# Performance work log

Hardware: AMD Instinct MI355X
Metric: run time of the kernel (lower is better)

Reference implementation:

```python
import jax, jax.numpy as jnp
import numpy as np

LAMBDA_RECON = 1.0
LAMBDA_IF = 0.5
LAMBDA_SMOOTH = 0.1

B, N, T = 8, 8, 262144


def setup_inputs() -> dict:
    key = jax.random.key(0)
    ks = jax.random.split(key, 7)
    return {
        "recon_real": jax.random.normal(ks[0], (B, T), dtype=jnp.float32),
        "recon_imag": jax.random.normal(ks[1], (B, T), dtype=jnp.float32),
        "target_real": jax.random.normal(ks[2], (B, T), dtype=jnp.float32),
        "target_imag": jax.random.normal(ks[3], (B, T), dtype=jnp.float32),
        "eIF": jax.random.normal(ks[4], (B, N, T), dtype=jnp.float32),
        "target_if": jax.random.normal(ks[5], (B, N, T), dtype=jnp.float32),
        "mode_mask": jax.random.randint(ks[6], (B, N), 0, 2, dtype=jnp.int32),
    }


def _mse(a, b):
    d = a - b
    return jnp.mean(d * d)


def reference(recon_real, recon_imag, target_real, target_imag, eIF, target_if, mode_mask):
    # reconstruction loss: MSE on real part + MSE on imag part
    recon_loss = _mse(recon_real, target_real) + _mse(recon_imag, target_imag)
    total_loss = LAMBDA_RECON * recon_loss

    # IF loss: mask broadcast over time axis, MSE of masked tensors
    maskf = (mode_mask == 1).astype(eIF.dtype)          # [B, N]
    valid = maskf[:, :, None]                            # [B, N, 1] broadcasts over T
    if_loss = _mse(eIF * valid, target_if * valid)
    total_loss = total_loss + LAMBDA_IF * if_loss

    # smoothness: mean of per-(b,n) mean squared temporal diff, over masked modes
    if_diff = eIF[:, :, 1:] - eIF[:, :, :-1]             # [B, N, T-1]
    per_mode = jnp.mean(if_diff * if_diff, axis=-1)      # [B, N]
    count = jnp.sum(maskf)
    smooth_loss = jnp.sum(per_mode * maskf) / jnp.maximum(count, 1.0)
    # original skips smooth term if no mode is active
    smooth_term = jnp.where(count > 0, LAMBDA_SMOOTH * smooth_loss, 0.0)
    total_loss = total_loss + smooth_term

    return total_loss, recon_loss, if_loss, smooth_loss
```

## Files before the change

kernel.cpp:

```cpp
#include <hip/hip_runtime.h>


namespace {
constexpr int    kB = 8;
constexpr int    kN = 8;
constexpr int    kT = 262144;
constexpr long long kBT  = (long long)kB * kT;
constexpr long long kBNT = (long long)kB * kN * kT;

constexpr int THREADS     = 256;
constexpr int RECON_UNITS = 512;
constexpr int SEGS        = 32;
constexpr int IF_UNITS    = kB * kN * SEGS;
constexpr int TOTAL_UNITS = RECON_UNITS + IF_UNITS;
constexpr int GRID        = 1024;

constexpr double LAMBDA_IF     = 0.5;
constexpr double LAMBDA_SMOOTH = 0.1;
}

__device__ __forceinline__ float sq(float x) { return x * x; }

__device__ __forceinline__ void block_reduce2_store(float a, float b, double* dst) {
    double da = (double)a, db = (double)b;
    #pragma unroll
    for (int o = 32; o > 0; o >>= 1) {
        da += __shfl_down(da, o, 64);
        db += __shfl_down(db, o, 64);
    }
    __shared__ double lds[8];
    const int lane = threadIdx.x & 63;
    const int wid  = threadIdx.x >> 6;
    if (lane == 0) { lds[wid] = da; lds[wid + 4] = db; }
    __syncthreads();
    if (threadIdx.x == 0) {
        dst[0] = lds[0] + lds[1] + lds[2] + lds[3];
        dst[1] = lds[4] + lds[5] + lds[6] + lds[7];
    }
    __syncthreads();
}

__global__ __launch_bounds__(THREADS, 4)
void vncmd_main_kernel(const float* __restrict__ rr, const float* __restrict__ ri,
                       const float* __restrict__ tr, const float* __restrict__ ti,
                       const float* __restrict__ eIF, const float* __restrict__ tIF,
                       const int* __restrict__ mask, double* __restrict__ ws) {
    const int tid = threadIdx.x;

    __shared__ int smask[kB * kN];
    if (tid < kB * kN) smask[tid] = mask[tid];
    __syncthreads();

    for (int u = blockIdx.x; u < TOTAL_UNITS; u += GRID) {
        if (u < RECON_UNITS) {
            constexpr int STRIDE = RECON_UNITS * THREADS;
            const int base = u * THREADS + tid;
            const float4* rr4 = (const float4*)rr;
            const float4* tr4 = (const float4*)tr;
            const float4* ri4 = (const float4*)ri;
            const float4* ti4 = (const float4*)ti;
            const int v0 = base, v1 = base + STRIDE, v2 = base + 2 * STRIDE, v3 = base + 3 * STRIDE;

            float4 x0 = rr4[v0], x1 = rr4[v1], x2 = rr4[v2], x3 = rr4[v3];
            float4 y0 = tr4[v0], y1 = tr4[v1], y2 = tr4[v2], y3 = tr4[v3];
            float4 u0 = ri4[v0], u1 = ri4[v1], u2 = ri4[v2], u3 = ri4[v3];
            float4 w0 = ti4[v0], w1 = ti4[v1], w2 = ti4[v2], w3 = ti4[v3];

            float a0 = sq(x0.x - y0.x) + sq(x0.y - y0.y) + sq(x0.z - y0.z) + sq(x0.w - y0.w)
                     + sq(x1.x - y1.x) + sq(x1.y - y1.y) + sq(x1.z - y1.z) + sq(x1.w - y1.w)
                     + sq(x2.x - y2.x) + sq(x2.y - y2.y) + sq(x2.z - y2.z) + sq(x2.w - y2.w)
                     + sq(x3.x - y3.x) + sq(x3.y - y3.y) + sq(x3.z - y3.z) + sq(x3.w - y3.w);
            float a1 = sq(u0.x - w0.x) + sq(u0.y - w0.y) + sq(u0.z - w0.z) + sq(u0.w - w0.w)
                     + sq(u1.x - w1.x) + sq(u1.y - w1.y) + sq(u1.z - w1.z) + sq(u1.w - w1.w)
                     + sq(u2.x - w2.x) + sq(u2.y - w2.y) + sq(u2.z - w2.z) + sq(u2.w - w2.w)
                     + sq(u3.x - w3.x) + sq(u3.y - w3.y) + sq(u3.z - w3.z) + sq(u3.w - w3.w);
            block_reduce2_store(a0, a1, ws + 2 * u);
        } else {
            const int iu  = u - RECON_UNITS;
            const int row = iu >> 5;
            const int seg = iu & (SEGS - 1);
            double* dst = ws + 2 * u;
            if (smask[row] != 1) {
                if (tid == 0) { dst[0] = 0.0; dst[1] = 0.0; }
                continue;
            }

            const float4* e4 = (const float4*)(eIF + (size_t)row * kT);
            const float4* t4 = (const float4*)(tIF + (size_t)row * kT);
            constexpr int VPR = kT / 4;
            constexpr int VPS = 2048;
            const int v0 = seg * VPS + tid;
            const bool lane63 = (tid & 63) == 63;

            float a2 = 0.f, a3 = 0.f;
            #pragma unroll
            for (int h = 0; h < 2; ++h) {
                const int b0 = v0 + (4 * h) * THREADS;
                const int b1 = b0 + THREADS, b2 = b0 + 2 * THREADS, b3 = b0 + 3 * THREADS;
                float4 e0 = e4[b0], e1 = e4[b1], e2 = e4[b2], e3 = e4[b3];
                float4 q0 = t4[b0], q1 = t4[b1], q2 = t4[b2], q3 = t4[b3];
                float n0 = 0.f, n1 = 0.f, n2 = 0.f, n3 = 0.f;
                if (lane63) {
                    n0 = (b0 + 1 < VPR) ? e4[b0 + 1].x : e0.w;
                    n1 = (b1 + 1 < VPR) ? e4[b1 + 1].x : e1.w;
                    n2 = (b2 + 1 < VPR) ? e4[b2 + 1].x : e2.w;
                    n3 = (b3 + 1 < VPR) ? e4[b3 + 1].x : e3.w;
                }
                a2 += sq(e0.x - q0.x) + sq(e0.y - q0.y) + sq(e0.z - q0.z) + sq(e0.w - q0.w)
                    + sq(e1.x - q1.x) + sq(e1.y - q1.y) + sq(e1.z - q1.z) + sq(e1.w - q1.w)
                    + sq(e2.x - q2.x) + sq(e2.y - q2.y) + sq(e2.z - q2.z) + sq(e2.w - q2.w)
                    + sq(e3.x - q3.x) + sq(e3.y - q3.y) + sq(e3.z - q3.z) + sq(e3.w - q3.w);
                a3 += sq(e0.y - e0.x) + sq(e0.z - e0.y) + sq(e0.w - e0.z)
                    + sq(e1.y - e1.x) + sq(e1.z - e1.y) + sq(e1.w - e1.z)
                    + sq(e2.y - e2.x) + sq(e2.z - e2.y) + sq(e2.w - e2.z)
                    + sq(e3.y - e3.x) + sq(e3.z - e3.y) + sq(e3.w - e3.z);
                float s0 = __shfl_down(e0.x, 1, 64);
                float s1 = __shfl_down(e1.x, 1, 64);
                float s2 = __shfl_down(e2.x, 1, 64);
                float s3 = __shfl_down(e3.x, 1, 64);
                if (lane63) { s0 = n0; s1 = n1; s2 = n2; s3 = n3; }
                a3 += sq(s0 - e0.w) + sq(s1 - e1.w) + sq(s2 - e2.w) + sq(s3 - e3.w);
            }
            block_reduce2_store(a2, a3, dst);
        }
    }
}

__global__ __launch_bounds__(THREADS)
void finalize_kernel(const double* __restrict__ ws,
                     const int* __restrict__ mask,
                     float* __restrict__ out) {
    const int tid = threadIdx.x;
    double s0 = 0.0, s1 = 0.0, s2 = 0.0, s3 = 0.0;
    #pragma unroll
    for (int k = 0; k < TOTAL_UNITS / THREADS; ++k) {
        const int i = k * THREADS + tid;
        double p = ws[2 * i], q = ws[2 * i + 1];
        if (i < RECON_UNITS) { s0 += p; s1 += q; }
        else                 { s2 += p; s3 += q; }
    }
    #pragma unroll
    for (int o = 32; o > 0; o >>= 1) {
        s0 += __shfl_down(s0, o, 64);
        s1 += __shfl_down(s1, o, 64);
        s2 += __shfl_down(s2, o, 64);
        s3 += __shfl_down(s3, o, 64);
    }
    __shared__ double lds[4][4];
    const int lane = tid & 63;
    const int wid  = tid >> 6;
    if (lane == 0) { lds[wid][0] = s0; lds[wid][1] = s1; lds[wid][2] = s2; lds[wid][3] = s3; }
    __syncthreads();
    if (tid == 0) {
        double t0 = lds[0][0] + lds[1][0] + lds[2][0] + lds[3][0];
        double t1 = lds[0][1] + lds[1][1] + lds[2][1] + lds[3][1];
        double t2 = lds[0][2] + lds[1][2] + lds[2][2] + lds[3][2];
        double t3 = lds[0][3] + lds[1][3] + lds[2][3] + lds[3][3];
        int c = 0;
        #pragma unroll
        for (int i = 0; i < kB * kN; ++i) c += (mask[i] == 1);
        double count = (double)c;
        double recon = t0 / (double)kBT + t1 / (double)kBT;
        double ifl   = t2 / (double)kBNT;
        double denom = (count > 1.0 ? count : 1.0) * (double)(kT - 1);
        double smooth = t3 / denom;
        double total = recon + LAMBDA_IF * ifl + (count > 0.0 ? LAMBDA_SMOOTH * smooth : 0.0);
        out[0] = (float)total;
        out[1] = (float)recon;
        out[2] = (float)ifl;
        out[3] = (float)smooth;
    }
}

extern "C" void kernel_launch(void* const* d_in, const int* in_sizes, int n_in,
                              void* d_out, int out_size, void* d_ws, size_t ws_size,
                              hipStream_t stream) {
    const float* rr  = (const float*)d_in[0];
    const float* ri  = (const float*)d_in[1];
    const float* tr  = (const float*)d_in[2];
    const float* ti  = (const float*)d_in[3];
    const float* eIF = (const float*)d_in[4];
    const float* tIF = (const float*)d_in[5];
    const int*   msk = (const int*)d_in[6];
    float* out = (float*)d_out;
    double* ws = (double*)d_ws;

    vncmd_main_kernel<<<GRID, THREADS, 0, stream>>>(
        rr, ri, tr, ti, eIF, tIF, msk, ws);
    finalize_kernel<<<1, THREADS, 0, stream>>>(ws, msk, out);
}
```

Before: 25.03 us.

## Give each block a fixed set of work units with one block reduction

Replaces the grid-stride loop, which ran a block reduction and barrier after every work unit, with a static assignment. Each block accumulates one recon unit plus two IF units, or two IF units, into registers and then does a single four-value block reduction. The finalize kernel now reads four doubles per block with vectorised double2 loads. This removes repeated LDS reductions and __syncthreads per block and shrinks the workspace, at the cost of a layout that is hard-coded to GRID=1024.

```diff
diff --git a/kernel.cpp b/kernel.cpp
--- a/kernel.cpp
+++ b/kernel.cpp
@@ -9,11 +9,8 @@
 constexpr long long kBNT = (long long)kB * kN * kT;
 
 constexpr int THREADS     = 256;
-constexpr int RECON_UNITS = 512;
+constexpr int GRID        = 1024;
 constexpr int SEGS        = 32;
-constexpr int IF_UNITS    = kB * kN * SEGS;
-constexpr int TOTAL_UNITS = RECON_UNITS + IF_UNITS;
-constexpr int GRID        = 1024;
 
 constexpr double LAMBDA_IF     = 0.5;
 constexpr double LAMBDA_SMOOTH = 0.1;
@@ -21,23 +18,73 @@
 
 __device__ __forceinline__ float sq(float x) { return x * x; }
 
-__device__ __forceinline__ void block_reduce2_store(float a, float b, double* dst) {
-    double da = (double)a, db = (double)b;
-    #pragma unroll
-    for (int o = 32; o > 0; o >>= 1) {
-        da += __shfl_down(da, o, 64);
-        db += __shfl_down(db, o, 64);
-    }
-    __shared__ double lds[8];
-    const int lane = threadIdx.x & 63;
-    const int wid  = threadIdx.x >> 6;
-    if (lane == 0) { lds[wid] = da; lds[wid + 4] = db; }
-    __syncthreads();
-    if (threadIdx.x == 0) {
-        dst[0] = lds[0] + lds[1] + lds[2] + lds[3];
-        dst[1] = lds[4] + lds[5] + lds[6] + lds[7];
-    }
-    __syncthreads();
+__device__ __forceinline__ void recon_accum(int u, int tid,
+                                            const float4* __restrict__ rr4,
+                                            const float4* __restrict__ tr4,
+                                            const float4* __restrict__ ri4,
+                                            const float4* __restrict__ ti4,
+                                            float& a0, float& a1) {
+    constexpr int STRIDE = 512 * THREADS;
+    const int base = u * THREADS + tid;
+    const int v0 = base, v1 = base + STRIDE, v2 = base + 2 * STRIDE, v3 = base + 3 * STRIDE;
+    float4 x0 = rr4[v0], x1 = rr4[v1], x2 = rr4[v2], x3 = rr4[v3];
+    float4 y0 = tr4[v0], y1 = tr4[v1], y2 = tr4[v2], y3 = tr4[v3];
+    float4 u0 = ri4[v0], u1 = ri4[v1], u2 = ri4[v2], u3 = ri4[v3];
+    float4 w0 = ti4[v0], w1 = ti4[v1], w2 = ti4[v2], w3 = ti4[v3];
+    a0 += sq(x0.x - y0.x) + sq(x0.y - y0.y) + sq(x0.z - y0.z) + sq(x0.w - y0.w)
+        + sq(x1.x - y1.x) + sq(x1.y - y1.y) + sq(x1.z - y1.z) + sq(x1.w - y1.w)
+        + sq(x2.x - y2.x) + sq(x2.y - y2.y) + sq(x2.z - y2.z) + sq(x2.w - y2.w)
+        + sq(x3.x - y3.x) + sq(x3.y - y3.y) + sq(x3.z - y3.z) + sq(x3.w - y3.w);
+    a1 += sq(u0.x - w0.x) + sq(u0.y - w0.y) + sq(u0.z - w0.z) + sq(u0.w - w0.w)
+        + sq(u1.x - w1.x) + sq(u1.y - w1.y) + sq(u1.z - w1.z) + sq(u1.w - w1.w)
+        + sq(u2.x - w2.x) + sq(u2.y - w2.y) + sq(u2.z - w2.z) + sq(u2.w - w2.w)
+        + sq(u3.x - w3.x) + sq(u3.y - w3.y) + sq(u3.z - w3.z) + sq(u3.w - w3.w);
+}
+
+__device__ __forceinline__ void if_accum(int iu, int tid,
+                                         const float* __restrict__ eIF,
+                                         const float* __restrict__ tIF,
+                                         const int* __restrict__ smask,
+                                         float& a2, float& a3) {
+    const int row = iu >> 5;
+    const int seg = iu & (SEGS - 1);
+    if (smask[row] != 1) return;
+
+    const float4* e4 = (const float4*)(eIF + (size_t)row * kT);
+    const float4* t4 = (const float4*)(tIF + (size_t)row * kT);
+    constexpr int VPR = kT / 4;
+    constexpr int VPS = 2048;
+    const int v0 = seg * VPS + tid;
+    const bool lane63 = (tid & 63) == 63;
+
+    #pragma unroll
+    for (int h = 0; h < 2; ++h) {
+        const int b0 = v0 + (4 * h) * THREADS;
+        const int b1 = b0 + THREADS, b2 = b0 + 2 * THREADS, b3 = b0 + 3 * THREADS;
+        float4 e0 = e4[b0], e1 = e4[b1], e2 = e4[b2], e3 = e4[b3];
+        float4 q0 = t4[b0], q1 = t4[b1], q2 = t4[b2], q3 = t4[b3];
+        float n0 = 0.f, n1 = 0.f, n2 = 0.f, n3 = 0.f;
+        if (lane63) {
+            n0 = (b0 + 1 < VPR) ? e4[b0 + 1].x : e0.w;
+            n1 = (b1 + 1 < VPR) ? e4[b1 + 1].x : e1.w;
+            n2 = (b2 + 1 < VPR) ? e4[b2 + 1].x : e2.w;
+            n3 = (b3 + 1 < VPR) ? e4[b3 + 1].x : e3.w;
+        }
+        a2 += sq(e0.x - q0.x) + sq(e0.y - q0.y) + sq(e0.z - q0.z) + sq(e0.w - q0.w)
+            + sq(e1.x - q1.x) + sq(e1.y - q1.y) + sq(e1.z - q1.z) + sq(e1.w - q1.w)
+            + sq(e2.x - q2.x) + sq(e2.y - q2.y) + sq(e2.z - q2.z) + sq(e2.w - q2.w)
+            + sq(e3.x - q3.x) + sq(e3.y - q3.y) + sq(e3.z - q3.z) + sq(e3.w - q3.w);
+        a3 += sq(e0.y - e0.x) + sq(e0.z - e0.y) + sq(e0.w - e0.z)
+            + sq(e1.y - e1.x) + sq(e1.z - e1.y) + sq(e1.w - e1.z)
+            + sq(e2.y - e2.x) + sq(e2.z - e2.y) + sq(e2.w - e2.z)
+            + sq(e3.y - e3.x) + sq(e3.z - e3.y) + sq(e3.w - e3.z);
+        float s0 = __shfl_down(e0.x, 1, 64);
+        float s1 = __shfl_down(e1.x, 1, 64);
+        float s2 = __shfl_down(e2.x, 1, 64);
+        float s3 = __shfl_down(e3.x, 1, 64);
+        if (lane63) { s0 = n0; s1 = n1; s2 = n2; s3 = n3; }
+        a3 += sq(s0 - e0.w) + sq(s1 - e1.w) + sq(s2 - e2.w) + sq(s3 - e3.w);
+    }
 }
 
 __global__ __launch_bounds__(THREADS, 4)
@@ -46,83 +93,46 @@
                        const float* __restrict__ eIF, const float* __restrict__ tIF,
                        const int* __restrict__ mask, double* __restrict__ ws) {
     const int tid = threadIdx.x;
+    const int bid = blockIdx.x;
 
     __shared__ int smask[kB * kN];
     if (tid < kB * kN) smask[tid] = mask[tid];
     __syncthreads();
 
-    for (int u = blockIdx.x; u < TOTAL_UNITS; u += GRID) {
-        if (u < RECON_UNITS) {
-            constexpr int STRIDE = RECON_UNITS * THREADS;
-            const int base = u * THREADS + tid;
-            const float4* rr4 = (const float4*)rr;
-            const float4* tr4 = (const float4*)tr;
-            const float4* ri4 = (const float4*)ri;
-            const float4* ti4 = (const float4*)ti;
-            const int v0 = base, v1 = base + STRIDE, v2 = base + 2 * STRIDE, v3 = base + 3 * STRIDE;
-
-            float4 x0 = rr4[v0], x1 = rr4[v1], x2 = rr4[v2], x3 = rr4[v3];
-            float4 y0 = tr4[v0], y1 = tr4[v1], y2 = tr4[v2], y3 = tr4[v3];
-            float4 u0 = ri4[v0], u1 = ri4[v1], u2 = ri4[v2], u3 = ri4[v3];
-            float4 w0 = ti4[v0], w1 = ti4[v1], w2 = ti4[v2], w3 = ti4[v3];
-
-            float a0 = sq(x0.x - y0.x) + sq(x0.y - y0.y) + sq(x0.z - y0.z) + sq(x0.w - y0.w)
-                     + sq(x1.x - y1.x) + sq(x1.y - y1.y) + sq(x1.z - y1.z) + sq(x1.w - y1.w)
-                     + sq(x2.x - y2.x) + sq(x2.y - y2.y) + sq(x2.z - y2.z) + sq(x2.w - y2.w)
-                     + sq(x3.x - y3.x) + sq(x3.y - y3.y) + sq(x3.z - y3.z) + sq(x3.w - y3.w);
-            float a1 = sq(u0.x - w0.x) + sq(u0.y - w0.y) + sq(u0.z - w0.z) + sq(u0.w - w0.w)
-                     + sq(u1.x - w1.x) + sq(u1.y - w1.y) + sq(u1.z - w1.z) + sq(u1.w - w1.w)
-                     + sq(u2.x - w2.x) + sq(u2.y - w2.y) + sq(u2.z - w2.z) + sq(u2.w - w2.w)
-                     + sq(u3.x - w3.x) + sq(u3.y - w3.y) + sq(u3.z - w3.z) + sq(u3.w - w3.w);
-            block_reduce2_store(a0, a1, ws + 2 * u);
-        } else {
-            const int iu  = u - RECON_UNITS;
-            const int row = iu >> 5;
-            const int seg = iu & (SEGS - 1);
-            double* dst = ws + 2 * u;
-            if (smask[row] != 1) {
-                if (tid == 0) { dst[0] = 0.0; dst[1] = 0.0; }
-                continue;
-            }
-
-            const float4* e4 = (const float4*)(eIF + (size_t)row * kT);
-            const float4* t4 = (const float4*)(tIF + (size_t)row * kT);
-            constexpr int VPR = kT / 4;
-            constexpr int VPS = 2048;
-            const int v0 = seg * VPS + tid;
-            const bool lane63 = (tid & 63) == 63;
-
-            float a2 = 0.f, a3 = 0.f;
-            #pragma unroll
-            for (int h = 0; h < 2; ++h) {
-                const int b0 = v0 + (4 * h) * THREADS;
-                const int b1 = b0 + THREADS, b2 = b0 + 2 * THREADS, b3 = b0 + 3 * THREADS;
-                float4 e0 = e4[b0], e1 = e4[b1], e2 = e4[b2], e3 = e4[b3];
-                float4 q0 = t4[b0], q1 = t4[b1], q2 = t4[b2], q3 = t4[b3];
-                float n0 = 0.f, n1 = 0.f, n2 = 0.f, n3 = 0.f;
-                if (lane63) {
-                    n0 = (b0 + 1 < VPR) ? e4[b0 + 1].x : e0.w;
-                    n1 = (b1 + 1 < VPR) ? e4[b1 + 1].x : e1.w;
-                    n2 = (b2 + 1 < VPR) ? e4[b2 + 1].x : e2.w;
-                    n3 = (b3 + 1 < VPR) ? e4[b3 + 1].x : e3.w;
-                }
-                a2 += sq(e0.x - q0.x) + sq(e0.y - q0.y) + sq(e0.z - q0.z) + sq(e0.w - q0.w)
-                    + sq(e1.x - q1.x) + sq(e1.y - q1.y) + sq(e1.z - q1.z) + sq(e1.w - q1.w)
-                    + sq(e2.x - q2.x) + sq(e2.y - q2.y) + sq(e2.z - q2.z) + sq(e2.w - q2.w)
-                    + sq(e3.x - q3.x) + sq(e3.y - q3.y) + sq(e3.z - q3.z) + sq(e3.w - q3.w);
-                a3 += sq(e0.y - e0.x) + sq(e0.z - e0.y) + sq(e0.w - e0.z)
-                    + sq(e1.y - e1.x) + sq(e1.z - e1.y) + sq(e1.w - e1.z)
-                    + sq(e2.y - e2.x) + sq(e2.z - e2.y) + sq(e2.w - e2.z)
-                    + sq(e3.y - e3.x) + sq(e3.z - e3.y) + sq(e3.w - e3.z);
-                float s0 = __shfl_down(e0.x, 1, 64);
-                float s1 = __shfl_down(e1.x, 1, 64);
-                float s2 = __shfl_down(e2.x, 1, 64);
-                float s3 = __shfl_down(e3.x, 1, 64);
-                if (lane63) { s0 = n0; s1 = n1; s2 = n2; s3 = n3; }
-                a3 += sq(s0 - e0.w) + sq(s1 - e1.w) + sq(s2 - e2.w) + sq(s3 - e3.w);
-            }
-            block_reduce2_store(a2, a3, dst);
-        }
+    const float4* rr4 = (const float4*)rr;
+    const float4* tr4 = (const float4*)tr;
+    const float4* ri4 = (const float4*)ri;
+    const float4* ti4 = (const float4*)ti;
+
+    float a0 = 0.f, a1 = 0.f, a2 = 0.f, a3 = 0.f;
+    if (bid < 512) {
+        recon_accum(bid, tid, rr4, tr4, ri4, ti4, a0, a1);
+        if_accum(bid + 512,  tid, eIF, tIF, smask, a2, a3);
+        if_accum(bid + 1536, tid, eIF, tIF, smask, a2, a3);
+    } else {
+        if_accum(bid - 512, tid, eIF, tIF, smask, a2, a3);
+        if_accum(bid + 512, tid, eIF, tIF, smask, a2, a3);
+    }
+
+    double d0 = (double)a0, d1 = (double)a1, d2 = (double)a2, d3 = (double)a3;
+    #pragma unroll
+    for (int o = 32; o > 0; o >>= 1) {
+        d0 += __shfl_down(d0, o, 64);
+        d1 += __shfl_down(d1, o, 64);
+        d2 += __shfl_down(d2, o, 64);
+        d3 += __shfl_down(d3, o, 64);
+    }
+    __shared__ double lds[4][4];
+    const int lane = tid & 63;
+    const int wid  = tid >> 6;
+    if (lane == 0) { lds[wid][0] = d0; lds[wid][1] = d1; lds[wid][2] = d2; lds[wid][3] = d3; }
+    __syncthreads();
+    if (tid == 0) {
+        double* dst = ws + 4 * bid;
+        dst[0] = lds[0][0] + lds[1][0] + lds[2][0] + lds[3][0];
+        dst[1] = lds[0][1] + lds[1][1] + lds[2][1] + lds[3][1];
+        dst[2] = lds[0][2] + lds[1][2] + lds[2][2] + lds[3][2];
+        dst[3] = lds[0][3] + lds[1][3] + lds[2][3] + lds[3][3];
     }
 }
 
@@ -131,13 +141,13 @@
                      const int* __restrict__ mask,
                      float* __restrict__ out) {
     const int tid = threadIdx.x;
+    const double2* w2 = (const double2*)ws;
     double s0 = 0.0, s1 = 0.0, s2 = 0.0, s3 = 0.0;
     #pragma unroll
-    for (int k = 0; k < TOTAL_UNITS / THREADS; ++k) {
-        const int i = k * THREADS + tid;
-        double p = ws[2 * i], q = ws[2 * i + 1];
-        if (i < RECON_UNITS) { s0 += p; s1 += q; }
-        else                 { s2 += p; s3 += q; }
+    for (int k = 0; k < GRID / THREADS; ++k) {
+        const int b = k * THREADS + tid;
+        double2 p = w2[2 * b], q = w2[2 * b + 1];
+        s0 += p.x; s1 += p.y; s2 += q.x; s3 += q.y;
     }
     #pragma unroll
     for (int o = 32; o > 0; o >>= 1) {
```

New measurement: 27.58 us. +10.2%, slower.
